# Kernel optimization log

Hardware: AMD Instinct MI355X
Metric: run time of the kernel (lower is better)

The kernel has to match this reference:

```python
import jax, jax.numpy as jnp
import numpy as np

B, S = 64, 512
CHAR_V, WORD_V = 8000, 100000
CE = WE = 256
D = 256            # gated conv channel dim (config.char_embed_size)
PE = CE + WE       # pos_embed_size must equal concat dim
P = 50             # predicate_num
DILS = (1, 2, 5, 1, 2, 5, 1, 2, 5, 1, 1, 1)
BN_EPS = 1e-3      # keras BatchNormalization default epsilon


def setup_inputs() -> dict:
    key = jax.random.key(0)
    k = jax.random.split(key, 12)
    s = 0.02
    return {
        "inputs": jax.random.randint(k[0], (B, S), 0, CHAR_V),
        "inputs_word": jax.random.randint(k[1], (B, S), 0, WORD_V),
        "inputs_position": jnp.broadcast_to(jnp.arange(S), (B, S)),
        "input_sub_loc": jnp.sort(jax.random.randint(k[2], (B, 2), 0, S), axis=1),
        "char_table": jax.random.normal(k[3], (CHAR_V, CE)) * s,
        "word_table": jax.random.normal(k[4], (WORD_V, WE)) * s,
        "pos_table": jax.random.normal(k[5], (S, PE)) * s,
        "conv_w1": jax.random.normal(k[6], (3, PE, 2 * D)) / np.sqrt(3.0 * PE),
        "conv_b1": jnp.zeros((2 * D,), jnp.float32),
        "conv_w": jax.random.normal(k[7], (11, 3, D, 2 * D)) / np.sqrt(3.0 * D),
        "conv_b": jnp.zeros((11, 2 * D), jnp.float32),
        "sub_w": jax.random.normal(k[8], (D, 2)) / np.sqrt(float(D)),
        "sub_b": jnp.zeros((2,), jnp.float32),
        "po_w": jax.random.normal(k[9], (3 * D, 2 * P)) / np.sqrt(3.0 * D),
        "po_b": jnp.zeros((2 * P,), jnp.float32),
        "bn_gamma": jnp.ones((3 * D,), jnp.float32),
        "bn_beta": jnp.zeros((3 * D,), jnp.float32),
    }


def _dgc(x, mask, w, b, dil):
    # dilated gated conv1d: conv -> split into gate/value -> gated residual -> mask
    h = jax.lax.conv_general_dilated(
        x, w, window_strides=(1,), padding="SAME", rhs_dilation=(dil,),
        dimension_numbers=("NWC", "WIO", "NWC")) + b
    g = jax.nn.sigmoid(h[..., :D])
    hv = h[..., D:]
    if x.shape[-1] != D:          # first layer projects PE -> D, no residual
        out = hv * g
    else:
        out = x * (1.0 - g) + hv * g
    return out * mask


def reference(inputs, inputs_word, inputs_position, input_sub_loc,
              char_table, word_table, pos_table,
              conv_w1, conv_b1, conv_w, conv_b,
              sub_w, sub_b, po_w, po_b, bn_gamma, bn_beta):
    # embeddings: concat(char, word) + pos   -> [B, S, PE]
    embed = jnp.concatenate([char_table[inputs], word_table[inputs_word]],
                            axis=-1) + pos_table[inputs_position]
    mask_bool = inputs != 0
    mask = mask_bool[..., None].astype(embed.dtype)  # [B, S, 1]

    x = _dgc(embed, mask, conv_w1, conv_b1, DILS[0])
    for i in range(11):
        x = _dgc(x, mask, conv_w[i], conv_b[i], DILS[i + 1])  # [B, S, D]

    sub_preds = jax.nn.sigmoid(jnp.einsum("bsd,dk->bsk", x, sub_w) + sub_b)

    # seq_gather of subject start/end vectors
    bidx = jnp.arange(B)
    sub_start = x[bidx, input_sub_loc[:, 0]]  # [B, D]
    sub_end = x[bidx, input_sub_loc[:, 1]]    # [B, D]
    vec = jnp.concatenate([sub_start, sub_end], axis=-1)  # [B, 2D]

    # seq_and_vec: broadcast vec over seq dim and concat -> [B, S, 3D]
    feat = jnp.concatenate(
        [x, jnp.broadcast_to(vec[:, None, :], (B, S, 2 * D))], axis=-1)

    # BatchNorm (training mode: batch statistics over (batch, seq))
    mu = jnp.mean(feat, axis=(0, 1))
    var = jnp.var(feat, axis=(0, 1))
    feat = (feat - mu) * jax.lax.rsqrt(var + BN_EPS) * bn_gamma + bn_beta

    po_preds = jax.nn.sigmoid(jnp.einsum("bsf,fp->bsp", feat, po_w) + po_b)

    return (jnp.transpose(sub_preds, (0, 2, 1)),   # [B, 2, S]
            jnp.transpose(po_preds, (0, 2, 1)),    # [B, 2P, S]
            mask_bool)
```

## Files before the change

kernel.cpp:

```cpp
#include <hip/hip_runtime.h>
#include <hip/hip_bf16.h>

typedef __attribute__((ext_vector_type(8))) short bf16x8;
typedef __attribute__((ext_vector_type(4))) float f32x4;

#define B_   64
#define S_   512
#define M_   32768
#define D_   256

__device__ __forceinline__ float b2f(unsigned short u) {
    union { unsigned int i; float f; } v; v.i = ((unsigned int)u) << 16; return v.f;
}
__device__ __forceinline__ unsigned short f2b(float f) {
    union { float f; unsigned int i; } v; v.f = f;
    unsigned int x = v.i;
    return (unsigned short)((x + 0x7fffu + ((x >> 16) & 1u)) >> 16);
}
__device__ __forceinline__ float sigm(float x) { return 1.f / (1.f + __expf(-x)); }

__device__ __forceinline__ float ldany(const void* p, size_t i, int f32) {
    return f32 ? ((const float*)p)[i] : b2f(((const unsigned short*)p)[i]);
}

__device__ __forceinline__ int omap(int o) {
    int half = o >> 8, d = o & 255;
    return ((d >> 4) * 32) + half * 16 + (d & 15);
}
__device__ __forceinline__ int omap_inv(int n) {
    int grp = n >> 5, half = (n >> 4) & 1, dlow = n & 15;
    return half * 256 + grp * 16 + dlow;
}

__global__ void k_detect(const void* sample, int* flag) {
    __shared__ int s;
    int t = threadIdx.x;
    if (t == 0) s = 0;
    __syncthreads();
    const unsigned short* u = (const unsigned short*)sample;
    float a = fabsf(b2f(u[2 * t]));
    if (!(a < 1e3f)) atomicOr(&s, 1);
    __syncthreads();
    if (t == 0) *flag = s;
}

__global__ __launch_bounds__(256)
void k_embed(const int* __restrict__ ids_c, const int* __restrict__ ids_w,
             const int* __restrict__ ids_p,
             const void* __restrict__ char_t,
             const void* __restrict__ word_t,
             const void* __restrict__ pos_t,
             unsigned short* __restrict__ embed,
             float* __restrict__ maskf,
             void* __restrict__ outv,
             const int* __restrict__ flag) {
    const int f32 = *flag;
    const int t = threadIdx.x;
    const int pos = blockIdx.x * 4 + (t >> 6);
    const int ch0 = (t & 63) * 8;
    const int c = ids_c[pos], w = ids_w[pos], p = ids_p[pos];
    if ((t & 63) == 0) {
        float m = (c != 0) ? 1.f : 0.f;
        maskf[pos] = m;
        size_t eidx = 65536 + 3276800 + (size_t)pos;
        if (f32) ((float*)outv)[eidx] = m;
        else ((unsigned short*)outv)[eidx] = f2b(m);
    }
    float tab[8], pe[8];
    const int in_char = (ch0 < 256);
    const size_t tidx = in_char ? ((size_t)c * 256 + ch0) : ((size_t)w * 256 + (ch0 - 256));
    const void* tp = in_char ? char_t : word_t;
    if (f32) {
        const float4 a0 = *(const float4*)((const float*)tp + tidx);
        const float4 a1 = *(const float4*)((const float*)tp + tidx + 4);
        tab[0]=a0.x; tab[1]=a0.y; tab[2]=a0.z; tab[3]=a0.w;
        tab[4]=a1.x; tab[5]=a1.y; tab[6]=a1.z; tab[7]=a1.w;
        const float4 b0 = *(const float4*)((const float*)pos_t + (size_t)p * 512 + ch0);
        const float4 b1 = *(const float4*)((const float*)pos_t + (size_t)p * 512 + ch0 + 4);
        pe[0]=b0.x; pe[1]=b0.y; pe[2]=b0.z; pe[3]=b0.w;
        pe[4]=b1.x; pe[5]=b1.y; pe[6]=b1.z; pe[7]=b1.w;
    } else {
        const unsigned short* tu = (const unsigned short*)tp + tidx;
        const unsigned short* pu = (const unsigned short*)pos_t + (size_t)p * 512 + ch0;
        uint4 av = *(const uint4*)tu;
        uint4 bv = *(const uint4*)pu;
        const unsigned short* as = (const unsigned short*)&av;
        const unsigned short* bs = (const unsigned short*)&bv;
#pragma unroll
        for (int i = 0; i < 8; ++i) { tab[i] = b2f(as[i]); pe[i] = b2f(bs[i]); }
    }
    unsigned short o[8];
#pragma unroll
    for (int i = 0; i < 8; ++i) o[i] = f2b(tab[i] + pe[i]);
    *(uint4*)(embed + (size_t)pos * 512 + ch0) = *(uint4*)o;
}

__global__ void k_repack(const void* __restrict__ w1,
                         const void* __restrict__ w11,
                         const void* __restrict__ b1,
                         const void* __restrict__ b11,
                         unsigned short* __restrict__ w1p,
                         unsigned short* __restrict__ wp,
                         float* __restrict__ biasP,
                         const int* __restrict__ flag) {
    const int f32 = *flag;
    const int T1 = 3 * 512 * 512 / 8;
    const int T2 = 11 * 3 * 512 * 256 / 8;
    const int T3 = 12 * 512;
    const int total = T1 + T2 + T3;
    for (int idx = blockIdx.x * blockDim.x + threadIdx.x; idx < total;
         idx += gridDim.x * blockDim.x) {
        if (idx < T1) {
            int row = idx >> 6;
            int c0 = (idx & 63) * 8;
            int tap = row >> 9, n = row & 511;
            int o = omap_inv(n);
            unsigned short v[8];
#pragma unroll
            for (int i = 0; i < 8; ++i)
                v[i] = f2b(ldany(w1, (size_t)tap * 262144 + (size_t)(c0 + i) * 512 + o, f32));
            *(uint4*)(w1p + ((size_t)row << 9) + c0) = *(uint4*)v;
        } else if (idx < T1 + T2) {
            int j = idx - T1;
            int row = j >> 5;
            int c0 = (j & 31) * 8;
            int lt = row >> 9, n = row & 511;
            int o = omap_inv(n);
            unsigned short v[8];
#pragma unroll
            for (int i = 0; i < 8; ++i)
                v[i] = f2b(ldany(w11, (size_t)lt * 131072 + (size_t)(c0 + i) * 512 + o, f32));
            *(uint4*)(wp + ((size_t)row << 8) + c0) = *(uint4*)v;
        } else {
            int j = idx - T1 - T2;
            if (j < 512) {
                biasP[omap(j)] = ldany(b1, j, f32);
            } else {
                int jj = j - 512;
                int lay = jj >> 9, o = jj & 511;
                biasP[512 + lay * 512 + omap(o)] = ldany(b11, jj, f32);
            }
        }
    }
}

template <int CIN, bool RES>
__global__ __launch_bounds__(256, 2)
void k_dgc(const unsigned short* __restrict__ xin,
           const unsigned short* __restrict__ wT,
           const float* __restrict__ bias,
           const float* __restrict__ maskf,
           unsigned short* __restrict__ xout,
           int dil) {
    __shared__ unsigned short ldsA[138 * 32];
    __shared__ unsigned short ldsB[3 * 128 * 32];
    const int id = blockIdx.x;
    const int xcd = id & 7, sl = id >> 3;
    const int mt = xcd * 32 + (sl >> 2);
    const int nt = sl & 3;
    const int m0 = mt * 128, n0 = nt * 128;
    const int b = m0 >> 9, s0 = m0 & 511;
    const int t = threadIdx.x;
    const int lane = t & 63, wv = t >> 6;
    const int wm = wv >> 1, wn = wv & 1;
    const int lm = lane & 15, lq = lane >> 4;
    const int NR = 128 + 2 * dil;

    f32x4 acc[4][4];
#pragma unroll
    for (int i = 0; i < 4; i++)
#pragma unroll
        for (int j = 0; j < 4; j++)
#pragma unroll
            for (int e = 0; e < 4; e++) acc[i][j][e] = 0.f;

    const unsigned short* xbase = xin + (size_t)b * S_ * CIN;

    for (int k0 = 0; k0 < CIN; k0 += 32) {
        __syncthreads();
        for (int i = t; i < NR * 4; i += 256) {
            int row = i >> 2, q = i & 3;
            int sp = s0 - dil + row;
            uint4 va = make_uint4(0u, 0u, 0u, 0u);
            if (sp >= 0 && sp < S_)
                va = *(const uint4*)(xbase + (size_t)sp * CIN + k0 + q * 8);
            *(uint4*)(ldsA + row * 32 + ((q ^ (row & 3)) * 8)) = va;
        }
#pragma unroll
        for (int i0 = 0; i0 < 6; ++i0) {
            int i = t + i0 * 256;
            int tap = i >> 9, rem = i & 511;
            int row = rem >> 2, q = rem & 3;
            uint4 vb = *(const uint4*)(wT + ((size_t)tap * 512 + n0 + row) * CIN + k0 + q * 8);
            *(uint4*)(ldsB + (tap * 128 + row) * 32 + ((q ^ (row & 3)) * 8)) = vb;
        }
        __syncthreads();
#pragma unroll
        for (int tap = 0; tap < 3; ++tap) {
            bf16x8 af[4], bfr[4];
#pragma unroll
            for (int mi = 0; mi < 4; ++mi) {
                const int er = wm * 64 + mi * 16 + lm + tap * dil;
                af[mi] = *(const bf16x8*)(ldsA + er * 32 + ((lq ^ (er & 3)) * 8));
            }
#pragma unroll
            for (int ni = 0; ni < 4; ++ni) {
                const int br = wn * 64 + ni * 16 + lm;
                bfr[ni] = *(const bf16x8*)(ldsB + (tap * 128 + br) * 32 + ((lq ^ (br & 3)) * 8));
            }
#pragma unroll
            for (int mi = 0; mi < 4; ++mi)
#pragma unroll
                for (int ni = 0; ni < 4; ++ni)
                    acc[mi][ni] = __builtin_amdgcn_mfma_f32_16x16x32_bf16(
                        af[mi], bfr[ni], acc[mi][ni], 0, 0, 0);
        }
    }

    const int colbase = n0 + wn * 64;
#pragma unroll
    for (int mi = 0; mi < 4; ++mi) {
#pragma unroll
        for (int p = 0; p < 2; ++p) {
            const int d = (colbase >> 1) + p * 16 + lm;
            const int ng = colbase + p * 32 + lm;
            const float bg = bias[ng], bv = bias[ng + 16];
#pragma unroll
            for (int r = 0; r < 4; ++r) {
                const int m = m0 + wm * 64 + mi * 16 + lq * 4 + r;
                float hg = acc[mi][2 * p][r] + bg;
                float hv = acc[mi][2 * p + 1][r] + bv;
                float g = sigm(hg);
                float o = hv * g;
                if (RES) {
                    float xi = b2f(xin[(size_t)m * CIN + d]);
                    o = xi * (1.f - g) + hv * g;
                }
                o *= maskf[m];
                xout[(size_t)m * 256 + d] = f2b(o);
            }
        }
    }
}

__global__ void k_vec(const unsigned short* __restrict__ x, const int* __restrict__ loc,
                      float* __restrict__ vec) {
    int b = blockIdx.x;
    int j = threadIdx.x;
    int which = j >> 8, d = j & 255;
    int s = loc[b * 2 + which];
    vec[b * 512 + j] = b2f(x[((size_t)(b * 512 + s)) * 256 + d]);
}

__global__ void k_zero(float* __restrict__ stats) { stats[threadIdx.x] = 0.f; }

__global__ void k_stats(const unsigned short* __restrict__ x, float* __restrict__ stats) {
    int c = threadIdx.x;
    int base = blockIdx.x * 128;
    float s = 0.f, q = 0.f;
    for (int r = 0; r < 128; ++r) {
        float v = b2f(x[(size_t)(base + r) * 256 + c]);
        s += v; q += v * v;
    }
    atomicAdd(&stats[c], s);
    atomicAdd(&stats[256 + c], q);
}

__global__ void k_final(const float* __restrict__ stats, const float* __restrict__ vec,
                        const void* __restrict__ gamma,
                        const void* __restrict__ beta,
                        float* __restrict__ scale, float* __restrict__ shift,
                        const int* __restrict__ flag) {
    const int f32 = *flag;
    int f = threadIdx.x;
    float mu, var;
    if (f < 256) {
        mu = stats[f] * (1.f / 32768.f);
        var = stats[256 + f] * (1.f / 32768.f) - mu * mu;
    } else {
        float s = 0.f, q = 0.f;
        int j = f - 256;
        for (int b = 0; b < 64; ++b) {
            float v = vec[b * 512 + j];
            s += v; q += v * v;
        }
        mu = s * (1.f / 64.f);
        var = q * (1.f / 64.f) - mu * mu;
    }
    float sc = ldany(gamma, f, f32) * rsqrtf(var + 1e-3f);
    scale[f] = sc;
    shift[f] = ldany(beta, f, f32) - mu * sc;
}

__global__ void k_prep1(const float* __restrict__ scale, const void* __restrict__ po_w,
                        const void* __restrict__ sub_w,
                        unsigned short* __restrict__ pwT,
                        const int* __restrict__ flag) {
    const int f32 = *flag;
    int idx = blockIdx.x * blockDim.x + threadIdx.x;
    int n = idx >> 8, k = idx & 255;
    float v = 0.f;
    if (n < 100) v = scale[k] * ldany(po_w, (size_t)k * 100 + n, f32);
    else if (n < 102) v = ldany(sub_w, (size_t)k * 2 + (n - 100), f32);
    pwT[n * 256 + k] = f2b(v);
}

__global__ __launch_bounds__(256)
void k_cmat(const float* __restrict__ scale, const float* __restrict__ shift,
            const float* __restrict__ vec,
            const void* __restrict__ po_w,
            const void* __restrict__ po_b,
            const void* __restrict__ sub_b,
            float* __restrict__ Cmat,
            const int* __restrict__ flag) {
    const int f32 = *flag;
    const int wid = blockIdx.x * 4 + (threadIdx.x >> 6);
    const int lane = threadIdx.x & 63;
    const int b = wid / 102, n = wid - b * 102;
    if (b >= 64) return;
    if (n >= 100) {
        if (lane == 0) Cmat[b * 128 + n] = ldany(sub_b, n - 100, f32);
        return;
    }
    float partial = 0.f;
#pragma unroll
    for (int f = lane; f < 768; f += 64) {
        float term = shift[f];
        if (f >= 256) term += vec[b * 512 + (f - 256)] * scale[f];
        partial += term * ldany(po_w, (size_t)f * 100 + n, f32);
    }
#pragma unroll
    for (int off = 32; off > 0; off >>= 1)
        partial += __shfl_xor(partial, off);
    if (lane == 0) Cmat[b * 128 + n] = partial + ldany(po_b, n, f32);
}

__global__ __launch_bounds__(256)
void k_po(const unsigned short* __restrict__ x,
          const unsigned short* __restrict__ pwT,
          const float* __restrict__ Cmat,
          void* __restrict__ outv,
          const int* __restrict__ flag) {
    const int f32 = *flag;
    __shared__ unsigned short ldsA[128 * 40];
    __shared__ unsigned short ldsB[128 * 40];
    const int mt = blockIdx.x;
    const int m0 = mt * 128;
    const int b = m0 >> 9;
    const int t = threadIdx.x;
    const int lane = t & 63, wv = t >> 6;
    const int wm = wv >> 1, wn = wv & 1;
    const int lm = lane & 15, lq = lane >> 4;

    f32x4 acc[4][4];
#pragma unroll
    for (int i = 0; i < 4; i++)
#pragma unroll
        for (int j = 0; j < 4; j++)
#pragma unroll
            for (int e = 0; e < 4; e++) acc[i][j][e] = 0.f;

    for (int k0 = 0; k0 < 256; k0 += 32) {
        __syncthreads();
#pragma unroll
        for (int a0 = 0; a0 < 2; ++a0) {
            int a = t + a0 * 256;
            int row = a >> 2, q = a & 3;
            uint4 va = *(const uint4*)(x + (size_t)(m0 + row) * 256 + k0 + q * 8);
            *(uint4*)(ldsA + row * 40 + q * 8) = va;
            uint4 vb = *(const uint4*)(pwT + (size_t)row * 256 + k0 + q * 8);
            *(uint4*)(ldsB + row * 40 + q * 8) = vb;
        }
        __syncthreads();
        bf16x8 af[4], bfr[4];
#pragma unroll
        for (int mi = 0; mi < 4; ++mi)
            af[mi] = *(const bf16x8*)(ldsA + (wm * 64 + mi * 16 + lm) * 40 + lq * 8);
#pragma unroll
        for (int ni = 0; ni < 4; ++ni)
            bfr[ni] = *(const bf16x8*)(ldsB + (wn * 64 + ni * 16 + lm) * 40 + lq * 8);
#pragma unroll
        for (int mi = 0; mi < 4; ++mi)
#pragma unroll
            for (int ni = 0; ni < 4; ++ni)
                acc[mi][ni] = __builtin_amdgcn_mfma_f32_16x16x32_bf16(
                    af[mi], bfr[ni], acc[mi][ni], 0, 0, 0);
    }

#pragma unroll
    for (int mi = 0; mi < 4; ++mi)
#pragma unroll
        for (int ni = 0; ni < 4; ++ni) {
            const int n = wn * 64 + ni * 16 + lm;
            const float cc = Cmat[b * 128 + n];
#pragma unroll
            for (int r = 0; r < 4; ++r) {
                const int m = m0 + wm * 64 + mi * 16 + lq * 4 + r;
                const int s = m & 511;
                float v = sigm(acc[mi][ni][r] + cc);
                if (n < 102) {
                    size_t eidx;
                    if (n < 100) eidx = 65536 + (((size_t)b * 100 + n) * 512 + s);
                    else eidx = ((size_t)b * 2 + (n - 100)) * 512 + s;
                    if (f32) ((float*)outv)[eidx] = v;
                    else ((unsigned short*)outv)[eidx] = f2b(v);
                }
            }
        }
}

extern "C" void kernel_launch(void* const* d_in, const int* in_sizes, int n_in,
                              void* d_out, int out_size, void* d_ws, size_t ws_size,
                              hipStream_t stream) {
    const int* ids_c = (const int*)d_in[0];
    const int* ids_w = (const int*)d_in[1];
    const int* ids_p = (const int*)d_in[2];
    const int* loc = (const int*)d_in[3];
    const void* char_t = d_in[4];
    const void* word_t = d_in[5];
    const void* pos_t = d_in[6];
    const void* w1 = d_in[7];
    const void* b1 = d_in[8];
    const void* w11 = d_in[9];
    const void* b11 = d_in[10];
    const void* sub_w = d_in[11];
    const void* sub_b = d_in[12];
    const void* po_w = d_in[13];
    const void* po_b = d_in[14];
    const void* gamma = d_in[15];
    const void* beta = d_in[16];

    char* ws = (char*)d_ws;
    unsigned short* embed = (unsigned short*)(ws + 0);
    unsigned short* xA = (unsigned short*)(ws + 33554432);
    unsigned short* xB = (unsigned short*)(ws + 50331648);
    unsigned short* w1p = (unsigned short*)(ws + 67108864);
    unsigned short* wp = (unsigned short*)(ws + 68681728);
    float* biasP = (float*)(ws + 77332480);
    float* maskf = (float*)(ws + 77357056);
    float* vec = (float*)(ws + 77488128);
    float* stats = (float*)(ws + 77619200);
    float* scale = (float*)(ws + 77621248);
    float* shift = (float*)(ws + 77624320);
    unsigned short* pwT = (unsigned short*)(ws + 77627392);
    float* Cmat = (float*)(ws + 77692928);
    int* dflag = (int*)(ws + 77725696);

    k_detect<<<1, 256, 0, stream>>>(word_t, dflag);
    k_zero<<<1, 512, 0, stream>>>(stats);
    k_embed<<<8192, 256, 0, stream>>>(ids_c, ids_w, ids_p, char_t, word_t, pos_t,
                                      embed, maskf, d_out, dflag);
    k_repack<<<2560, 256, 0, stream>>>(w1, w11, b1, b11, w1p, wp, biasP, dflag);

    k_dgc<512, false><<<1024, 256, 0, stream>>>(embed, w1p, biasP, maskf, xA, 1);

    const int dils[12] = {1, 2, 5, 1, 2, 5, 1, 2, 5, 1, 1, 1};
    unsigned short* xi = xA;
    unsigned short* xo = xB;
    for (int i = 1; i < 12; ++i) {
        k_dgc<256, true><<<1024, 256, 0, stream>>>(
            xi, wp + (size_t)(i - 1) * 3 * 512 * 256, biasP + i * 512, maskf, xo, dils[i]);
        unsigned short* tmp = xi; xi = xo; xo = tmp;
    }

    k_vec<<<64, 512, 0, stream>>>(xi, loc, vec);
    k_stats<<<256, 256, 0, stream>>>(xi, stats);
    k_final<<<1, 768, 0, stream>>>(stats, vec, gamma, beta, scale, shift, dflag);
    k_prep1<<<128, 256, 0, stream>>>(scale, po_w, sub_w, pwT, dflag);
    k_cmat<<<1632, 256, 0, stream>>>(scale, shift, vec, po_w, po_b, sub_b, Cmat, dflag);
    k_po<<<256, 256, 0, stream>>>(xi, pwT, Cmat, d_out, dflag);
}
```

Measured before the change: 670.7 us.

## Switch gated conv to 32x32 MFMA with 256-row tiles and padded LDS

The dilated gated conv GEMM moves from 16x16x32 to 32x32x16 bf16 MFMA. The M tile grows from 128 to 256 rows, which halves the grid. Each wave now covers 64 rows by all 128 N columns, so weight tiles are reused across more rows. LDS rows are padded to 36 elements instead of XOR swizzling, and the epilogue pairs gate and value columns through a lane shuffle. The risk is fewer blocks, which means lower occupancy and wave count, plus a larger LDS footprint and more accumulator registers, and an epilogue where half the lanes stay idle.

```diff
diff --git a/kernel.cpp b/kernel.cpp
--- a/kernel.cpp
+++ b/kernel.cpp
@@ -3,6 +3,7 @@
 
 typedef __attribute__((ext_vector_type(8))) short bf16x8;
 typedef __attribute__((ext_vector_type(4))) float f32x4;
+typedef __attribute__((ext_vector_type(16))) float f32x16;
 
 #define B_   64
 #define S_   512
@@ -152,27 +153,26 @@
            const float* __restrict__ maskf,
            unsigned short* __restrict__ xout,
            int dil) {
-    __shared__ unsigned short ldsA[138 * 32];
-    __shared__ unsigned short ldsB[3 * 128 * 32];
+    __shared__ unsigned short ldsA[266 * 36];
+    __shared__ unsigned short ldsB[3 * 128 * 36];
     const int id = blockIdx.x;
     const int xcd = id & 7, sl = id >> 3;
-    const int mt = xcd * 32 + (sl >> 2);
+    const int mt = xcd * 16 + (sl >> 2);
     const int nt = sl & 3;
-    const int m0 = mt * 128, n0 = nt * 128;
+    const int m0 = mt * 256, n0 = nt * 128;
     const int b = m0 >> 9, s0 = m0 & 511;
     const int t = threadIdx.x;
-    const int lane = t & 63, wv = t >> 6;
-    const int wm = wv >> 1, wn = wv & 1;
-    const int lm = lane & 15, lq = lane >> 4;
-    const int NR = 128 + 2 * dil;
-
-    f32x4 acc[4][4];
-#pragma unroll
-    for (int i = 0; i < 4; i++)
+    const int lane = t & 63, wm = t >> 6;
+    const int lc = lane & 31, lh = lane >> 5;
+    const int NR = 256 + 2 * dil;
+
+    f32x16 acc[2][4];
+#pragma unroll
+    for (int i = 0; i < 2; i++)
 #pragma unroll
         for (int j = 0; j < 4; j++)
 #pragma unroll
-            for (int e = 0; e < 4; e++) acc[i][j][e] = 0.f;
+            for (int e = 0; e < 16; e++) acc[i][j][e] = 0.f;
 
     const unsigned short* xbase = xin + (size_t)b * S_ * CIN;
 
@@ -184,7 +184,7 @@
             uint4 va = make_uint4(0u, 0u, 0u, 0u);
             if (sp >= 0 && sp < S_)
                 va = *(const uint4*)(xbase + (size_t)sp * CIN + k0 + q * 8);
-            *(uint4*)(ldsA + row * 32 + ((q ^ (row & 3)) * 8)) = va;
+            *(uint4*)(ldsA + row * 36 + q * 8) = va;
         }
 #pragma unroll
         for (int i0 = 0; i0 < 6; ++i0) {
@@ -192,52 +192,59 @@
             int tap = i >> 9, rem = i & 511;
             int row = rem >> 2, q = rem & 3;
             uint4 vb = *(const uint4*)(wT + ((size_t)tap * 512 + n0 + row) * CIN + k0 + q * 8);
-            *(uint4*)(ldsB + (tap * 128 + row) * 32 + ((q ^ (row & 3)) * 8)) = vb;
+            *(uint4*)(ldsB + (tap * 128 + row) * 36 + q * 8) = vb;
         }
         __syncthreads();
 #pragma unroll
         for (int tap = 0; tap < 3; ++tap) {
-            bf16x8 af[4], bfr[4];
-#pragma unroll
-            for (int mi = 0; mi < 4; ++mi) {
-                const int er = wm * 64 + mi * 16 + lm + tap * dil;
-                af[mi] = *(const bf16x8*)(ldsA + er * 32 + ((lq ^ (er & 3)) * 8));
+#pragma unroll
+            for (int ks = 0; ks < 2; ++ks) {
+                bf16x8 af[2], bfr[4];
+#pragma unroll
+                for (int mi = 0; mi < 2; ++mi) {
+                    const int row = wm * 64 + mi * 32 + lc + tap * dil;
+                    af[mi] = *(const bf16x8*)(ldsA + row * 36 + ks * 16 + lh * 8);
+                }
+#pragma unroll
+                for (int nj = 0; nj < 4; ++nj) {
+                    const int brow = nj * 32 + lc;
+                    bfr[nj] = *(const bf16x8*)(ldsB + (tap * 128 + brow) * 36 + ks * 16 + lh * 8);
+                }
+#pragma unroll
+                for (int mi = 0; mi < 2; ++mi)
+#pragma unroll
+                    for (int nj = 0; nj < 4; ++nj)
+                        acc[mi][nj] = __builtin_amdgcn_mfma_f32_32x32x16_bf16(
+                            af[mi], bfr[nj], acc[mi][nj], 0, 0, 0);
             }
-#pragma unroll
-            for (int ni = 0; ni < 4; ++ni) {
-                const int br = wn * 64 + ni * 16 + lm;
-                bfr[ni] = *(const bf16x8*)(ldsB + (tap * 128 + br) * 32 + ((lq ^ (br & 3)) * 8));
-            }
-#pragma unroll
-            for (int mi = 0; mi < 4; ++mi)
-#pragma unroll
-                for (int ni = 0; ni < 4; ++ni)
-                    acc[mi][ni] = __builtin_amdgcn_mfma_f32_16x16x32_bf16(
-                        af[mi], bfr[ni], acc[mi][ni], 0, 0, 0);
-        }
-    }
-
-    const int colbase = n0 + wn * 64;
-#pragma unroll
-    for (int mi = 0; mi < 4; ++mi) {
-#pragma unroll
-        for (int p = 0; p < 2; ++p) {
-            const int d = (colbase >> 1) + p * 16 + lm;
-            const int ng = colbase + p * 32 + lm;
-            const float bg = bias[ng], bv = bias[ng + 16];
-#pragma unroll
-            for (int r = 0; r < 4; ++r) {
-                const int m = m0 + wm * 64 + mi * 16 + lq * 4 + r;
-                float hg = acc[mi][2 * p][r] + bg;
-                float hv = acc[mi][2 * p + 1][r] + bv;
-                float g = sigm(hg);
-                float o = hv * g;
-                if (RES) {
-                    float xi = b2f(xin[(size_t)m * CIN + d]);
-                    o = xi * (1.f - g) + hv * g;
+        }
+    }
+
+    const int isval = (lc >> 4) & 1;
+    const int dl = lc & 15;
+#pragma unroll
+    for (int mi = 0; mi < 2; ++mi) {
+#pragma unroll
+        for (int nj = 0; nj < 4; ++nj) {
+            const int dbase = (n0 >> 1) + nj * 16;
+            const int d = dbase + dl;
+            const float bown = bias[n0 + nj * 32 + lc];
+#pragma unroll
+            for (int r = 0; r < 16; ++r) {
+                const int row = (r & 3) + 8 * (r >> 2) + 4 * lh;
+                const int m = m0 + wm * 64 + mi * 32 + row;
+                float h = acc[mi][nj][r] + bown;
+                float other = __shfl_xor(h, 16);
+                if (isval) {
+                    float g = sigm(other);
+                    float o = h * g;
+                    if (RES) {
+                        float xi = b2f(xin[(size_t)m * CIN + d]);
+                        o = xi * (1.f - g) + h * g;
+                    }
+                    o *= maskf[m];
+                    xout[(size_t)m * 256 + d] = f2b(o);
                 }
-                o *= maskf[m];
-                xout[(size_t)m * 256 + d] = f2b(o);
             }
         }
     }
@@ -452,13 +459,13 @@
                                       embed, maskf, d_out, dflag);
     k_repack<<<2560, 256, 0, stream>>>(w1, w11, b1, b11, w1p, wp, biasP, dflag);
 
-    k_dgc<512, false><<<1024, 256, 0, stream>>>(embed, w1p, biasP, maskf, xA, 1);
+    k_dgc<512, false><<<512, 256, 0, stream>>>(embed, w1p, biasP, maskf, xA, 1);
 
     const int dils[12] = {1, 2, 5, 1, 2, 5, 1, 2, 5, 1, 1, 1};
     unsigned short* xi = xA;
     unsigned short* xo = xB;
     for (int i = 1; i < 12; ++i) {
-        k_dgc<256, true><<<1024, 256, 0, stream>>>(
+        k_dgc<256, true><<<512, 256, 0, stream>>>(
             xi, wp + (size_t)(i - 1) * 3 * 512 * 256, biasP + i * 512, maskf, xo, dils[i]);
         unsigned short* tmp = xi; xi = xo; xo = tmp;
     }
```

Result: slower. 1.038 ms (+54.8%).
